# Optimization experiments

Hardware: AMD Instinct MI355X
Metric: run time of the kernel (lower is better)

The kernel has to match this reference:

```python
import jax, jax.numpy as jnp
import numpy as np

B, S, T, H, E, V = 64, 512, 12, 256, 256, 50000


def _xavier(key, shape):
    lim = np.sqrt(6.0 / (shape[0] + shape[1]))
    return jax.random.uniform(key, shape, jnp.float32, -lim, lim)


def setup_inputs() -> dict:
    key = jax.random.key(0)
    ks = jax.random.split(key, 14)
    return {
        "input_ids": jax.random.randint(ks[0], (B, S), 0, V),
        "tree_ids": jax.random.randint(ks[1], (B, T, S), 0, S),
        "tree_ids_r": jax.random.randint(ks[2], (B, T, S), 0, S),
        "tree_ids_l": jax.random.randint(ks[3], (B, T, S), 0, S),
        "emb": _xavier(ks[4], (V, E)),
        "W_ioux": _xavier(ks[5], (E, 3 * H)),
        "b_ioux": jnp.zeros((3 * H,), jnp.float32),
        "U_iou_r": _xavier(ks[6], (H, 3 * H)),
        "U_iou_l": _xavier(ks[7], (H, 3 * H)),
        "W_f": _xavier(ks[8], (E, H)),
        "b_f": jnp.zeros((H,), jnp.float32),
        "U_f0": _xavier(ks[9], (H, H)),
        "U_f1": _xavier(ks[10], (H, H)),
        "U_f2": _xavier(ks[11], (H, H)),
        "U_f3": _xavier(ks[12], (H, H)),
    }


def reference(input_ids, tree_ids, tree_ids_r, tree_ids_l, emb,
              W_ioux, b_ioux, U_iou_r, U_iou_l, W_f, b_f,
              U_f0, U_f1, U_f2, U_f3):
    x = emb[input_ids]                      # [B, S, E]
    Bn, Sn = x.shape[0], x.shape[1]
    Hn = U_f0.shape[0]
    bidx = jnp.arange(Bn)[:, None]          # [B, 1] batch index for scatter

    def take(a, idx):                       # gather along node dim: out[b,s]=a[b,idx[b,s]]
        return jnp.take_along_axis(a, idx[..., None], axis=1)

    iou_x = x @ W_ioux + b_ioux             # precompute; constant across steps
    f_x = x @ W_f + b_f

    def step(carry, ids):
        h, c = carry
        td, tr, tl = ids                    # each [B, S]
        # which parent nodes receive children this step (node 0 excluded)
        counts = jnp.zeros((Bn, Sn), x.dtype).at[bidx, td].add(1.0)
        mask = (counts.at[:, 0].set(0.0) > 0)[..., None]  # [B, S, 1]
        # scatter-add child hidden projections into parent iou preactivations
        iou = iou_x.at[bidx, tr].add(h @ U_iou_r)
        iou = iou.at[bidx, tl].add(h @ U_iou_l)
        i, o, u = jnp.split(iou, 3, axis=-1)
        i, o, u = jax.nn.sigmoid(i), jax.nn.sigmoid(o), jnp.tanh(u)
        # forget gate per child: gather parent fx and child-hidden projections
        f = jax.nn.sigmoid(take(f_x, td)
                           + take(h @ U_f0 + h @ U_f1, tr)
                           + take(h @ U_f2 + h @ U_f3, tl))
        c_new = (i * u).at[bidx, td].add(f * c)
        h_new = o * jnp.tanh(c_new)
        h = jnp.where(mask, h_new, h)
        c = jnp.where(mask, c_new, c)
        return (h, c), None

    h0 = jnp.zeros((Bn, Sn, Hn), x.dtype)
    ids = (jnp.swapaxes(tree_ids, 0, 1),
           jnp.swapaxes(tree_ids_r, 0, 1),
           jnp.swapaxes(tree_ids_l, 0, 1))   # [T, B, S]
    (h, c), _ = jax.lax.scan(step, (h0, h0), ids)

    roots = tree_ids[:, -1, :].max(axis=1)   # [B]
    h_root = h[jnp.arange(Bn), roots]        # [B, H]
    return h, c, h_root
```

## Files before the change

kernel.cpp:

```cpp
#include <hip/hip_runtime.h>
#include <stdint.h>

#define B_ 64
#define S_ 512
#define T_ 12
#define M_ (B_*S_)
#define NP_ 2048

typedef __attribute__((ext_vector_type(8))) short bf16x8;
typedef __attribute__((ext_vector_type(4))) float f32x4;

__device__ __forceinline__ uint16_t f2bf(float f){
  union { float f; uint32_t u; } x; x.f = f;
  uint32_t r = x.u + 0x7FFFu + ((x.u >> 16) & 1u);
  return (uint16_t)(r >> 16);
}
__device__ __forceinline__ float bf2f(uint16_t u){
  union { float f; uint32_t u; } x; x.u = ((uint32_t)u) << 16; return x.f;
}
__device__ __forceinline__ float sigm(float x){ return 1.0f/(1.0f + expf(-x)); }
__device__ __forceinline__ float4 bf4(const uint16_t* p){
  const ushort4 v = *reinterpret_cast<const ushort4*>(p);
  return make_float4(bf2f(v.x), bf2f(v.y), bf2f(v.z), bf2f(v.w));
}

__device__ __forceinline__ void gload16(const uint16_t* g, uint16_t* l){
  __builtin_amdgcn_global_load_lds(
      (const __attribute__((address_space(1))) uint32_t*)g,
      (__attribute__((address_space(3))) uint32_t*)l, 16, 0, 0);
}

__global__ void zero16(uint4* __restrict__ p, long n16){
  const long i = (long)blockIdx.x * 256 + threadIdx.x;
  if (i < n16) p[i] = make_uint4(0,0,0,0);
}
__global__ void bf16_to_f32(const uint16_t* __restrict__ src, float* __restrict__ dst, long n){
  const long i = ((long)blockIdx.x * 256 + threadIdx.x) * 4;
  if (i + 3 < n) {
    const float4 o = bf4(src + i);
    *reinterpret_cast<float4*>(dst + i) = o;
  }
}

__global__ void build_ucatT(const float* __restrict__ Ur, const float* __restrict__ Ul,
                            const float* __restrict__ f0, const float* __restrict__ f1,
                            const float* __restrict__ f2, const float* __restrict__ f3,
                            uint16_t* __restrict__ UcatT){
  const int idx = blockIdx.x * 256 + threadIdx.x;
  const int n = idx >> 8, k = idx & 255;
  float v;
  if (n < 768)        v = Ur[k*768 + n];
  else if (n < 1536)  v = Ul[k*768 + (n-768)];
  else if (n < 1792) { int j = n-1536; v = f0[k*256+j] + f1[k*256+j]; }
  else               { int j = n-1792; v = f2[k*256+j] + f3[k*256+j]; }
  UcatT[(long)n*256 + k] = f2bf(v);
}

__global__ void build_wallT(const float* __restrict__ Wioux, const float* __restrict__ Wf,
                            uint16_t* __restrict__ WT){
  const int idx = blockIdx.x * 256 + threadIdx.x;
  const int n = idx >> 8, k = idx & 255;
  const float v = (n < 768) ? Wioux[(long)k*768 + n] : Wf[(long)k*256 + (n-768)];
  WT[(long)n*256 + k] = f2bf(v);
}

__global__ __launch_bounds__(256)
void mfma_gemm(const float* __restrict__ Af, const int* __restrict__ row_ids,
               const uint16_t* __restrict__ BT,
               const float* __restrict__ bias, const float* __restrict__ bias2, int split,
               uint16_t* __restrict__ C, int N)
{
  __shared__ uint16_t As[128][40];
  __shared__ uint16_t Bs[128][40];
  const int tid  = threadIdx.x;
  const int lane = tid & 63;
  const int wave = tid >> 6;
  const int wr = wave >> 1, wc = wave & 1;
  const int id = blockIdx.x, rx = id & 7, q = id >> 3;
  const int mt = rx + 8*(q >> 3);
  const int nt = q & 7;
  const long m0 = (long)mt * 128;
  const int  n0 = nt * 128;

  const int srow = tid >> 1;
  const int sseg = (tid & 1) * 16;
  const long arid = (long)row_ids[m0 + srow];

  f32x4 acc[4][4];
  #pragma unroll
  for (int i=0;i<4;i++)
    #pragma unroll
    for (int j=0;j<4;j++) acc[i][j] = (f32x4){0.f,0.f,0.f,0.f};

  for (int ks = 0; ks < 256; ks += 32) {
    {
      const float* sf = Af + arid*256 + ks + sseg;
      uint16_t tmp[16];
      #pragma unroll
      for (int e=0;e<16;e++) tmp[e] = f2bf(sf[e]);
      *reinterpret_cast<uint4*>(&As[srow][sseg])     = *reinterpret_cast<const uint4*>(&tmp[0]);
      *reinterpret_cast<uint4*>(&As[srow][sseg + 8]) = *reinterpret_cast<const uint4*>(&tmp[8]);
    }
    {
      const uint16_t* src = BT + (long)(n0 + srow)*256 + ks + sseg;
      *reinterpret_cast<uint4*>(&Bs[srow][sseg])     = *reinterpret_cast<const uint4*>(src);
      *reinterpret_cast<uint4*>(&Bs[srow][sseg + 8]) = *reinterpret_cast<const uint4*>(src + 8);
    }
    __syncthreads();

    bf16x8 af[4], bfv[4];
    #pragma unroll
    for (int i=0;i<4;i++)
      af[i] = *reinterpret_cast<const bf16x8*>(&As[wr*64 + i*16 + (lane & 15)][(lane >> 4)*8]);
    #pragma unroll
    for (int j=0;j<4;j++)
      bfv[j] = *reinterpret_cast<const bf16x8*>(&Bs[wc*64 + j*16 + (lane & 15)][(lane >> 4)*8]);
    #pragma unroll
    for (int i=0;i<4;i++)
      #pragma unroll
      for (int j=0;j<4;j++)
        acc[i][j] = __builtin_amdgcn_mfma_f32_16x16x32_bf16(af[i], bfv[j], acc[i][j], 0, 0, 0);
    __syncthreads();
  }

  const int col16 = lane & 15, rquad = lane >> 4;
  #pragma unroll
  for (int j=0;j<4;j++){
    const int col = n0 + wc*64 + j*16 + col16;
    const float bv = (col < split) ? bias[col] : bias2[col - split];
    #pragma unroll
    for (int i=0;i<4;i++){
      const long rbase = m0 + wr*64 + i*16 + rquad*4;
      #pragma unroll
      for (int r=0;r<4;r++)
        C[(rbase + r)*N + col] = f2bf(acc[i][j][r] + bv);
    }
  }
}

__global__ __launch_bounds__(256)
void gemm_step(const uint16_t* __restrict__ A, const uint16_t* __restrict__ BT,
               uint16_t* __restrict__ C, int N)
{
  __shared__ __align__(16) uint16_t As[2][4096];
  __shared__ __align__(16) uint16_t Bs[2][4096];
  const int tid = threadIdx.x, lane = tid & 63, wave = tid >> 6;
  const int wr = wave >> 1, wc = wave & 1;
  const int id = blockIdx.x, rx = id & 7, q = id >> 3;
  const int mt = rx + 8*(q >> 4);
  const int nt = q & 15;
  const long m0 = (long)mt * 128;
  const int  n0 = nt * 128;

  const int rl0 = wave*32 + (lane >> 2);
  const int rl1 = rl0 + 16;
  const int sg0 = (lane & 3) ^ ((rl0 >> 1) & 3);
  const int sg1 = (lane & 3) ^ ((rl1 >> 1) & 3);
  const uint16_t* ga0 = A + (m0 + rl0)*256 + sg0*8;
  const uint16_t* ga1 = A + (m0 + rl1)*256 + sg1*8;
  const uint16_t* gb0 = BT + (long)(n0 + rl0)*256 + sg0*8;
  const uint16_t* gb1 = BT + (long)(n0 + rl1)*256 + sg1*8;

  f32x4 acc[4][4];
  #pragma unroll
  for (int i=0;i<4;i++)
    #pragma unroll
    for (int j=0;j<4;j++) acc[i][j] = (f32x4){0.f,0.f,0.f,0.f};

  const int l15 = lane & 15, lseg = lane >> 4;
  int aoff[4], boff[4];
  #pragma unroll
  for (int i=0;i<4;i++){ const int m = wr*64 + i*16 + l15; aoff[i] = m*32 + ((lseg ^ ((m>>1)&3))<<3); }
  #pragma unroll
  for (int j=0;j<4;j++){ const int n = wc*64 + j*16 + l15; boff[j] = n*32 + ((lseg ^ ((n>>1)&3))<<3); }

  {
    uint16_t* a = &As[0][wave*1024];
    uint16_t* b = &Bs[0][wave*1024];
    gload16(ga0, a); gload16(ga1, a + 512);
    gload16(gb0, b); gload16(gb1, b + 512);
  }
  asm volatile("s_waitcnt vmcnt(0)" ::: "memory");
  __builtin_amdgcn_s_barrier();

  #pragma unroll
  for (int tt = 0; tt < 8; ++tt) {
    if (tt < 7) {
      const int nb = (tt + 1) & 1;
      const int ks = (tt + 1) * 32;
      uint16_t* a = &As[nb][wave*1024];
      uint16_t* b = &Bs[nb][wave*1024];
      gload16(ga0 + ks, a); gload16(ga1 + ks, a + 512);
      gload16(gb0 + ks, b); gload16(gb1 + ks, b + 512);
    }
    const int cb = tt & 1;
    bf16x8 af[4], bfv[4];
    #pragma unroll
    for (int i=0;i<4;i++) af[i]  = *reinterpret_cast<const bf16x8*>(&As[cb][aoff[i]]);
    #pragma unroll
    for (int j=0;j<4;j++) bfv[j] = *reinterpret_cast<const bf16x8*>(&Bs[cb][boff[j]]);
    #pragma unroll
    for (int i=0;i<4;i++)
      #pragma unroll
      for (int j=0;j<4;j++)
        acc[i][j] = __builtin_amdgcn_mfma_f32_16x16x32_bf16(af[i], bfv[j], acc[i][j], 0, 0, 0);
    if (tt < 7) {
      asm volatile("s_waitcnt vmcnt(0)" ::: "memory");
      __builtin_amdgcn_s_barrier();
    }
  }

  const int rquad = lane >> 4;
  #pragma unroll
  for (int j=0;j<4;j++){
    const int col = n0 + wc*64 + j*16 + l15;
    #pragma unroll
    for (int i=0;i<4;i++){
      const long rbase = m0 + wr*64 + i*16 + rquad*4;
      #pragma unroll
      for (int r=0;r<4;r++)
        C[(rbase + r)*N + col] = f2bf(acc[i][j][r]);
    }
  }
}

__global__ void build_csr(const int* __restrict__ td_g, const int* __restrict__ tr_g,
                          const int* __restrict__ tl_g,
                          int* __restrict__ csr_off, int* __restrict__ csr_val){
  const int t = blockIdx.x >> 6;
  const int b = blockIdx.x & 63;
  __shared__ int ids[S_];
  __shared__ int cnt[S_];
  __shared__ int off[S_];
  __shared__ int chc[8][S_];
  const int s = threadIdx.x;
  const int q = s >> 6;
  const int* srcs[3] = {td_g, tr_g, tl_g};
  for (int arr = 0; arr < 3; ++arr) {
    const int myid = srcs[arr][((long)b*T_ + t)*S_ + s];
    ids[s] = myid;
    cnt[s] = 0;
    #pragma unroll
    for (int qq=0; qq<8; qq++) chc[qq][s] = 0;
    __syncthreads();
    atomicAdd(&cnt[myid], 1);
    atomicAdd(&chc[q][myid], 1);
    __syncthreads();
    int rank = 0;
    for (int qq = 0; qq < q; ++qq) rank += chc[qq][myid];
    for (int i = q*64; i < s; ++i) rank += (ids[i] == myid) ? 1 : 0;
    off[s] = cnt[s];
    __syncthreads();
    for (int w = 1; w < S_; w <<= 1){
      const int v = (s >= w) ? off[s-w] : 0;
      __syncthreads();
      off[s] += v;
      __syncthreads();
    }
    const long base = (((long)arr*T_ + t)*B_ + b);
    int* offs = csr_off + base*(S_+1);
    int* vals = csr_val + base*S_;
    offs[s] = off[s] - cnt[s];
    if (s == S_-1) offs[S_] = off[s];
    vals[(off[myid] - cnt[myid]) + rank] = s;
    __syncthreads();
  }
}

__global__ __launch_bounds__(256)
void step_update(uint16_t* __restrict__ h,
                 const uint16_t* __restrict__ c_in, uint16_t* __restrict__ c_out,
                 const uint16_t* __restrict__ P,
                 const uint16_t* __restrict__ ioufx,
                 const int* __restrict__ csr_off, const int* __restrict__ csr_val,
                 const int* __restrict__ tr_g, const int* __restrict__ tl_g,
                 int t, int row0)
{
  const int wave = threadIdx.x >> 6, lane = threadIdx.x & 63;
  const int id = blockIdx.x, rx = id & 7, q = id >> 3;
  const int b_local = rx + 8*(q >> 7);
  const int rg = q & 127;
  const long bs = (long)row0 + b_local*512 + rg*4 + wave;
  const int b = (int)(bs >> 9), s = (int)(bs & 511);
  const int j = lane * 4;

  const int* off_td = csr_off + (((long)0*T_ + t)*B_ + b)*(S_+1);
  const int td0 = off_td[s], td1 = off_td[s+1];
  const bool masked = (s != 0) && (td1 > td0);
  if (!masked) {
    *reinterpret_cast<ushort4*>(c_out + bs*256 + j) =
        *reinterpret_cast<const ushort4*>(c_in + bs*256 + j);
    return;
  }
  const int* off_tr = csr_off + (((long)1*T_ + t)*B_ + b)*(S_+1);
  const int* off_tl = csr_off + (((long)2*T_ + t)*B_ + b)*(S_+1);
  const int* val_td = csr_val + (((long)0*T_ + t)*B_ + b)*S_;
  const int* val_tr = csr_val + (((long)1*T_ + t)*B_ + b)*S_;
  const int* val_tl = csr_val + (((long)2*T_ + t)*B_ + b)*S_;

  const long lbase = (long)(b<<9) - row0;

  const long ib = bs*1024;
  float4 ai = bf4(ioufx + ib + j);
  float4 ao = bf4(ioufx + ib + 256 + j);
  float4 au = bf4(ioufx + ib + 512 + j);
  for (int p = off_tr[s]; p < off_tr[s+1]; ++p) {
    const long pr = (lbase + val_tr[p]) * NP_;
    const float4 x = bf4(P + pr + j), y = bf4(P + pr + 256 + j), z = bf4(P + pr + 512 + j);
    ai.x+=x.x; ai.y+=x.y; ai.z+=x.z; ai.w+=x.w;
    ao.x+=y.x; ao.y+=y.y; ao.z+=y.z; ao.w+=y.w;
    au.x+=z.x; au.y+=z.y; au.z+=z.z; au.w+=z.w;
  }
  for (int p = off_tl[s]; p < off_tl[s+1]; ++p) {
    const long pr = (lbase + val_tl[p]) * NP_;
    const float4 x = bf4(P + pr + 768 + j), y = bf4(P + pr + 1024 + j), z = bf4(P + pr + 1280 + j);
    ai.x+=x.x; ai.y+=x.y; ai.z+=x.z; ai.w+=x.w;
    ao.x+=y.x; ao.y+=y.y; ao.z+=y.z; ao.w+=y.w;
    au.x+=z.x; au.y+=z.y; au.z+=z.z; au.w+=z.w;
  }
  float4 cacc;
  cacc.x = sigm(ai.x)*tanhf(au.x); cacc.y = sigm(ai.y)*tanhf(au.y);
  cacc.z = sigm(ai.z)*tanhf(au.z); cacc.w = sigm(ai.w)*tanhf(au.w);
  const float4 fxv = bf4(ioufx + ib + 768 + j);
  const int* trrow = tr_g + ((long)b*T_ + t)*S_;
  const int* tlrow = tl_g + ((long)b*T_ + t)*S_;
  for (int p = td0; p < td1; ++p) {
    const int sp = val_td[p];
    const long prr = (lbase + trrow[sp]) * NP_ + 1536;
    const long prl = (lbase + tlrow[sp]) * NP_ + 1792;
    const float4 pa = bf4(P + prr + j), pb = bf4(P + prl + j);
    const float4 cv = bf4(c_in + ((long)(b<<9) + sp)*256 + j);
    cacc.x += sigm(fxv.x + pa.x + pb.x) * cv.x;
    cacc.y += sigm(fxv.y + pa.y + pb.y) * cv.y;
    cacc.z += sigm(fxv.z + pa.z + pb.z) * cv.z;
    cacc.w += sigm(fxv.w + pa.w + pb.w) * cv.w;
  }
  ushort4 ho, co;
  ho.x = f2bf(sigm(ao.x) * tanhf(cacc.x));
  ho.y = f2bf(sigm(ao.y) * tanhf(cacc.y));
  ho.z = f2bf(sigm(ao.z) * tanhf(cacc.z));
  ho.w = f2bf(sigm(ao.w) * tanhf(cacc.w));
  co.x = f2bf(cacc.x); co.y = f2bf(cacc.y); co.z = f2bf(cacc.z); co.w = f2bf(cacc.w);
  *reinterpret_cast<ushort4*>(h + bs*256 + j) = ho;
  *reinterpret_cast<ushort4*>(c_out + bs*256 + j) = co;
}

__global__ void root_kernel(const uint16_t* __restrict__ h, const int* __restrict__ td_g,
                            float* __restrict__ out_root){
  const int b = blockIdx.x;
  __shared__ int red[256];
  const int* td = td_g + ((long)b*T_ + (T_-1))*S_;
  int m = 0;
  for (int s = threadIdx.x; s < S_; s += 256) m = max(m, td[s]);
  red[threadIdx.x] = m; __syncthreads();
  for (int w = 128; w > 0; w >>= 1){
    if (threadIdx.x < w) red[threadIdx.x] = max(red[threadIdx.x], red[threadIdx.x+w]);
    __syncthreads();
  }
  const int root = red[0];
  out_root[b*256 + threadIdx.x] = bf2f(h[((long)b*512 + root)*256 + threadIdx.x]);
}

extern "C" void kernel_launch(void* const* d_in, const int* in_sizes, int n_in,
                              void* d_out, int out_size, void* d_ws, size_t ws_size,
                              hipStream_t stream) {
  const int*   input_ids  = (const int*)  d_in[0];
  const int*   tree_ids   = (const int*)  d_in[1];
  const int*   tree_ids_r = (const int*)  d_in[2];
  const int*   tree_ids_l = (const int*)  d_in[3];
  const float* emb        = (const float*)d_in[4];
  const float* W_ioux     = (const float*)d_in[5];
  const float* b_ioux     = (const float*)d_in[6];
  const float* W_f        = (const float*)d_in[9];
  const float* b_f        = (const float*)d_in[10];
  float* out = (float*)d_out;

  size_t woff = 0;
  auto alloc = [&](size_t bytes)->char*{
    char* p = (char*)d_ws + woff; woff += (bytes + 255) & ~(size_t)255; return p;
  };
  uint16_t* ioufx  = (uint16_t*)alloc((size_t)M_*1024*2);
  uint16_t* hA     = (uint16_t*)alloc((size_t)M_*256*2);
  uint16_t* cA     = (uint16_t*)alloc((size_t)M_*256*2);
  uint16_t* cB     = (uint16_t*)alloc((size_t)M_*256*2);
  int* csr_off     = (int*)     alloc((size_t)3*T_*B_*(S_+1)*4);
  int* csr_val     = (int*)     alloc((size_t)3*T_*B_*S_*4);
  uint16_t* UcatT  = (uint16_t*)alloc((size_t)NP_*256*2);
  uint16_t* WallT  = (uint16_t*)alloc((size_t)1024*256*2);
  const int CB = 32;
  uint16_t* P      = (uint16_t*)alloc((size_t)CB*S_*NP_*2);

  build_ucatT<<<2048, 256, 0, stream>>>((const float*)d_in[7], (const float*)d_in[8],
      (const float*)d_in[11], (const float*)d_in[12], (const float*)d_in[13], (const float*)d_in[14],
      UcatT);
  build_wallT<<<1024, 256, 0, stream>>>(W_ioux, W_f, WallT);
  mfma_gemm<<<2048, 256, 0, stream>>>(emb, input_ids, WallT, b_ioux, b_f, 768, ioufx, 1024);
  build_csr<<<T_*B_, S_, 0, stream>>>(tree_ids, tree_ids_r, tree_ids_l, csr_off, csr_val);
  zero16<<<8192, 256, 0, stream>>>((uint4*)hA, 2097152L);

  uint16_t *cc = cA, *cn = cB;
  for (int t = 0; t < T_; ++t) {
    for (int b0 = 0; b0 < B_; b0 += CB) {
      const int row0 = b0 * S_;
      gemm_step<<<2048, 256, 0, stream>>>(hA + (long)row0*256, UcatT, P, NP_);
      step_update<<<4096, 256, 0, stream>>>(hA, cc, cn, P, ioufx,
                                            csr_off, csr_val, tree_ids_r, tree_ids_l,
                                            t, row0);
    }
    uint16_t* tc = cc; cc = cn; cn = tc;
  }

  bf16_to_f32<<<8192, 256, 0, stream>>>(hA, out, (long)M_*256);
  bf16_to_f32<<<8192, 256, 0, stream>>>(cc, out + (long)M_*256, (long)M_*256);
  root_kernel<<<B_, 256, 0, stream>>>(hA, tree_ids, out + 2L*M_*256);
}
```

Baseline: 1.321 ms.

## Special-case first step, reuse pipelined GEMM for embedding projection, enlarge batch chunk

Because h and c start at zero, step 0 needs no recurrent GEMM or scatter, so a dedicated t0_update kernel computes h and c directly from the precomputed input projections. The embedding rows are first gathered into a bf16 buffer, and the initial projection then runs through the double-buffered gemm_pipe kernel instead of the older unpipelined fp32-converting GEMM. The per-step chunk size grows from 32 to up to 64 batches, depending on workspace, to cut launch count. Risks: the larger P buffer must fit in the workspace, and zero16 now also clears the adjacent c buffer that t0 relies on.

```diff
diff --git a/kernel.cpp b/kernel.cpp
--- a/kernel.cpp
+++ b/kernel.cpp
@@ -64,91 +64,28 @@
   WT[(long)n*256 + k] = f2bf(v);
 }
 
+__global__ void gather_embg(const float* __restrict__ emb, const int* __restrict__ ids,
+                            uint16_t* __restrict__ out){
+  const int wave = threadIdx.x >> 6, lane = threadIdx.x & 63;
+  const long row = (long)blockIdx.x*4 + wave;
+  const long rid = (long)ids[row];
+  const float4 v = *reinterpret_cast<const float4*>(emb + rid*256 + lane*4);
+  ushort4 o; o.x=f2bf(v.x); o.y=f2bf(v.y); o.z=f2bf(v.z); o.w=f2bf(v.w);
+  *reinterpret_cast<ushort4*>(out + row*256 + lane*4) = o;
+}
+
 __global__ __launch_bounds__(256)
-void mfma_gemm(const float* __restrict__ Af, const int* __restrict__ row_ids,
-               const uint16_t* __restrict__ BT,
+void gemm_pipe(const uint16_t* __restrict__ A, const uint16_t* __restrict__ BT,
                const float* __restrict__ bias, const float* __restrict__ bias2, int split,
-               uint16_t* __restrict__ C, int N)
-{
-  __shared__ uint16_t As[128][40];
-  __shared__ uint16_t Bs[128][40];
-  const int tid  = threadIdx.x;
-  const int lane = tid & 63;
-  const int wave = tid >> 6;
-  const int wr = wave >> 1, wc = wave & 1;
-  const int id = blockIdx.x, rx = id & 7, q = id >> 3;
-  const int mt = rx + 8*(q >> 3);
-  const int nt = q & 7;
-  const long m0 = (long)mt * 128;
-  const int  n0 = nt * 128;
-
-  const int srow = tid >> 1;
-  const int sseg = (tid & 1) * 16;
-  const long arid = (long)row_ids[m0 + srow];
-
-  f32x4 acc[4][4];
-  #pragma unroll
-  for (int i=0;i<4;i++)
-    #pragma unroll
-    for (int j=0;j<4;j++) acc[i][j] = (f32x4){0.f,0.f,0.f,0.f};
-
-  for (int ks = 0; ks < 256; ks += 32) {
-    {
-      const float* sf = Af + arid*256 + ks + sseg;
-      uint16_t tmp[16];
-      #pragma unroll
-      for (int e=0;e<16;e++) tmp[e] = f2bf(sf[e]);
-      *reinterpret_cast<uint4*>(&As[srow][sseg])     = *reinterpret_cast<const uint4*>(&tmp[0]);
-      *reinterpret_cast<uint4*>(&As[srow][sseg + 8]) = *reinterpret_cast<const uint4*>(&tmp[8]);
-    }
-    {
-      const uint16_t* src = BT + (long)(n0 + srow)*256 + ks + sseg;
-      *reinterpret_cast<uint4*>(&Bs[srow][sseg])     = *reinterpret_cast<const uint4*>(src);
-      *reinterpret_cast<uint4*>(&Bs[srow][sseg + 8]) = *reinterpret_cast<const uint4*>(src + 8);
-    }
-    __syncthreads();
-
-    bf16x8 af[4], bfv[4];
-    #pragma unroll
-    for (int i=0;i<4;i++)
-      af[i] = *reinterpret_cast<const bf16x8*>(&As[wr*64 + i*16 + (lane & 15)][(lane >> 4)*8]);
-    #pragma unroll
-    for (int j=0;j<4;j++)
-      bfv[j] = *reinterpret_cast<const bf16x8*>(&Bs[wc*64 + j*16 + (lane & 15)][(lane >> 4)*8]);
-    #pragma unroll
-    for (int i=0;i<4;i++)
-      #pragma unroll
-      for (int j=0;j<4;j++)
-        acc[i][j] = __builtin_amdgcn_mfma_f32_16x16x32_bf16(af[i], bfv[j], acc[i][j], 0, 0, 0);
-    __syncthreads();
-  }
-
-  const int col16 = lane & 15, rquad = lane >> 4;
-  #pragma unroll
-  for (int j=0;j<4;j++){
-    const int col = n0 + wc*64 + j*16 + col16;
-    const float bv = (col < split) ? bias[col] : bias2[col - split];
-    #pragma unroll
-    for (int i=0;i<4;i++){
-      const long rbase = m0 + wr*64 + i*16 + rquad*4;
-      #pragma unroll
-      for (int r=0;r<4;r++)
-        C[(rbase + r)*N + col] = f2bf(acc[i][j][r] + bv);
-    }
-  }
-}
-
-__global__ __launch_bounds__(256)
-void gemm_step(const uint16_t* __restrict__ A, const uint16_t* __restrict__ BT,
-               uint16_t* __restrict__ C, int N)
+               uint16_t* __restrict__ C, int N, int NT)
 {
   __shared__ __align__(16) uint16_t As[2][4096];
   __shared__ __align__(16) uint16_t Bs[2][4096];
   const int tid = threadIdx.x, lane = tid & 63, wave = tid >> 6;
   const int wr = wave >> 1, wc = wave & 1;
   const int id = blockIdx.x, rx = id & 7, q = id >> 3;
-  const int mt = rx + 8*(q >> 4);
-  const int nt = q & 15;
+  const int mt = rx + 8*(q / NT);
+  const int nt = q % NT;
   const long m0 = (long)mt * 128;
   const int  n0 = nt * 128;
 
@@ -214,12 +151,13 @@
   #pragma unroll
   for (int j=0;j<4;j++){
     const int col = n0 + wc*64 + j*16 + l15;
+    const float bv = bias ? ((col < split) ? bias[col] : bias2[col - split]) : 0.0f;
     #pragma unroll
     for (int i=0;i<4;i++){
       const long rbase = m0 + wr*64 + i*16 + rquad*4;
       #pragma unroll
       for (int r=0;r<4;r++)
-        C[(rbase + r)*N + col] = f2bf(acc[i][j][r]);
+        C[(rbase + r)*N + col] = f2bf(acc[i][j][r] + bv);
     }
   }
 }
@@ -268,6 +206,31 @@
 }
 
 __global__ __launch_bounds__(256)
+void t0_update(uint16_t* __restrict__ h, uint16_t* __restrict__ c_out,
+               const uint16_t* __restrict__ ioufx, const int* __restrict__ csr_off)
+{
+  const int wave = threadIdx.x >> 6, lane = threadIdx.x & 63;
+  const long bs = (long)blockIdx.x*4 + wave;
+  const int b = (int)(bs >> 9), s = (int)(bs & 511);
+  const int j = lane * 4;
+  const int* off_td = csr_off + (long)b*(S_+1);
+  if (s == 0 || off_td[s+1] <= off_td[s]) return;
+  const long ib = bs*1024;
+  const float4 ai = bf4(ioufx + ib + j);
+  const float4 ao = bf4(ioufx + ib + 256 + j);
+  const float4 au = bf4(ioufx + ib + 512 + j);
+  float4 cacc;
+  cacc.x = sigm(ai.x)*tanhf(au.x); cacc.y = sigm(ai.y)*tanhf(au.y);
+  cacc.z = sigm(ai.z)*tanhf(au.z); cacc.w = sigm(ai.w)*tanhf(au.w);
+  ushort4 ho, co;
+  ho.x = f2bf(sigm(ao.x)*tanhf(cacc.x)); ho.y = f2bf(sigm(ao.y)*tanhf(cacc.y));
+  ho.z = f2bf(sigm(ao.z)*tanhf(cacc.z)); ho.w = f2bf(sigm(ao.w)*tanhf(cacc.w));
+  co.x = f2bf(cacc.x); co.y = f2bf(cacc.y); co.z = f2bf(cacc.z); co.w = f2bf(cacc.w);
+  *reinterpret_cast<ushort4*>(h + bs*256 + j) = ho;
+  *reinterpret_cast<ushort4*>(c_out + bs*256 + j) = co;
+}
+
+__global__ __launch_bounds__(256)
 void step_update(uint16_t* __restrict__ h,
                  const uint16_t* __restrict__ c_in, uint16_t* __restrict__ c_out,
                  const uint16_t* __restrict__ P,
@@ -387,25 +350,32 @@
   int* csr_val     = (int*)     alloc((size_t)3*T_*B_*S_*4);
   uint16_t* UcatT  = (uint16_t*)alloc((size_t)NP_*256*2);
   uint16_t* WallT  = (uint16_t*)alloc((size_t)1024*256*2);
-  const int CB = 32;
+  int CB = 64;
+  while (CB > 8 && woff + (size_t)CB*S_*NP_*2 > ws_size) CB >>= 1;
   uint16_t* P      = (uint16_t*)alloc((size_t)CB*S_*NP_*2);
+  uint16_t* embg   = P;
 
   build_ucatT<<<2048, 256, 0, stream>>>((const float*)d_in[7], (const float*)d_in[8],
       (const float*)d_in[11], (const float*)d_in[12], (const float*)d_in[13], (const float*)d_in[14],
       UcatT);
   build_wallT<<<1024, 256, 0, stream>>>(W_ioux, W_f, WallT);
-  mfma_gemm<<<2048, 256, 0, stream>>>(emb, input_ids, WallT, b_ioux, b_f, 768, ioufx, 1024);
+  gather_embg<<<M_/4, 256, 0, stream>>>(emb, input_ids, embg);
+  gemm_pipe<<<(M_/128)*8, 256, 0, stream>>>(embg, WallT, b_ioux, b_f, 768, ioufx, 1024, 8);
   build_csr<<<T_*B_, S_, 0, stream>>>(tree_ids, tree_ids_r, tree_ids_l, csr_off, csr_val);
-  zero16<<<8192, 256, 0, stream>>>((uint4*)hA, 2097152L);
+  zero16<<<12288, 256, 0, stream>>>((uint4*)hA, 3145728L);
 
   uint16_t *cc = cA, *cn = cB;
-  for (int t = 0; t < T_; ++t) {
+  t0_update<<<M_/4, 256, 0, stream>>>(hA, cn, ioufx, csr_off);
+  { uint16_t* tc = cc; cc = cn; cn = tc; }
+  for (int t = 1; t < T_; ++t) {
     for (int b0 = 0; b0 < B_; b0 += CB) {
       const int row0 = b0 * S_;
-      gemm_step<<<2048, 256, 0, stream>>>(hA + (long)row0*256, UcatT, P, NP_);
-      step_update<<<4096, 256, 0, stream>>>(hA, cc, cn, P, ioufx,
-                                            csr_off, csr_val, tree_ids_r, tree_ids_l,
-                                            t, row0);
+      const int Mc   = CB * S_;
+      gemm_pipe<<<(Mc/128)*16, 256, 0, stream>>>(hA + (long)row0*256, UcatT,
+                                                 nullptr, nullptr, 0, P, NP_, 16);
+      step_update<<<CB*128, 256, 0, stream>>>(hA, cc, cn, P, ioufx,
+                                              csr_off, csr_val, tree_ids_r, tree_ids_l,
+                                              t, row0);
     }
     uint16_t* tc = cc; cc = cn; cn = tc;
   }
```

Measured after the change: 1.179 ms. -10.8%, faster.
